# Kernel optimization log

Measured on AMD Instinct MI355X. Metric: run time of the kernel, lower is better.

Reference implementation:

```python
import jax, jax.numpy as jnp
import numpy as np

HIDDEN = 4096
N_HEADS = 32
N_KV = 8
HEAD_DIM = 128
ROPE_BASE = 10000.0


def setup_inputs() -> dict:
    key = jax.random.key(0)
    k0, k1, k2, k3, k4 = jax.random.split(key, 5)
    B, S = 1, 2048
    scale = 0.02
    return {
        "hidden_states": jax.random.normal(k0, (B, S, HIDDEN), dtype=jnp.float32),
        "Wq": jax.random.normal(k1, (N_HEADS * HEAD_DIM, HIDDEN), dtype=jnp.float32) * scale,
        "Wk": jax.random.normal(k2, (N_KV * HEAD_DIM, HIDDEN), dtype=jnp.float32) * scale,
        "Wv": jax.random.normal(k3, (N_KV * HEAD_DIM, HIDDEN), dtype=jnp.float32) * scale,
        "Wo": jax.random.normal(k4, (HIDDEN, N_HEADS * HEAD_DIM), dtype=jnp.float32) * scale,
    }


def _rotate_half(x):
    x1, x2 = jnp.split(x, 2, axis=-1)
    return jnp.concatenate([-x2, x1], axis=-1)


def _rope_cos_sin(seq_len, dtype):
    inv_freq = 1.0 / (ROPE_BASE ** (jnp.arange(0, HEAD_DIM, 2, dtype=jnp.float32) / HEAD_DIM))
    t = jnp.arange(seq_len, dtype=jnp.float32)
    freqs = jnp.outer(t, inv_freq)                 # [S, hd/2]
    emb = jnp.concatenate([freqs, freqs], axis=-1) # [S, hd]
    return jnp.cos(emb).astype(dtype), jnp.sin(emb).astype(dtype)


def reference(hidden_states, Wq, Wk, Wv, Wo):
    B, S, _ = hidden_states.shape
    scale = HEAD_DIM ** -0.5
    groups = N_HEADS // N_KV

    q = (hidden_states @ Wq.T).reshape(B, S, N_HEADS, HEAD_DIM).transpose(0, 2, 1, 3)
    k = (hidden_states @ Wk.T).reshape(B, S, N_KV, HEAD_DIM).transpose(0, 2, 1, 3)
    v = (hidden_states @ Wv.T).reshape(B, S, N_KV, HEAD_DIM).transpose(0, 2, 1, 3)

    cos, sin = _rope_cos_sin(S, q.dtype)           # [S, hd] each, broadcast over (B, H)
    q = q * cos + _rotate_half(q) * sin
    k = k * cos + _rotate_half(k) * sin

    # repeat_kv: [B, nkv, S, hd] -> [B, nkv*groups, S, hd]
    k = jnp.broadcast_to(k[:, :, None], (B, N_KV, groups, S, HEAD_DIM)).reshape(B, N_HEADS, S, HEAD_DIM)
    v = jnp.broadcast_to(v[:, :, None], (B, N_KV, groups, S, HEAD_DIM)).reshape(B, N_HEADS, S, HEAD_DIM)

    scores = jnp.einsum('bhqd,bhkd->bhqk', q, k) * scale
    causal = jnp.tril(jnp.ones((S, S), dtype=bool))
    scores = jnp.where(causal, scores, -jnp.inf)
    probs = jax.nn.softmax(scores.astype(jnp.float32), axis=-1).astype(q.dtype)

    attn = jnp.einsum('bhqk,bhkd->bhqd', probs, v)            # [B, H, S, hd]
    attn = attn.transpose(0, 2, 1, 3).reshape(B, S, N_HEADS * HEAD_DIM)
    return attn @ Wo.T
```

## Files before the change

### kernel.cpp

```cpp
#include <hip/hip_runtime.h>
#include <hip/hip_bf16.h>
#include <math.h>

#define S_LEN 2048
#define HIDDEN 4096
#define N_HEADS 32
#define N_KV 8
#define HEAD_DIM 128

typedef __attribute__((ext_vector_type(8))) short short8;
typedef __attribute__((ext_vector_type(4))) float f32x4;

typedef __attribute__((address_space(3))) unsigned int as3_u32;
typedef const __attribute__((address_space(1))) unsigned int as1_u32;

__device__ __forceinline__ void gload16(const void* g, void* lds) {
  __builtin_amdgcn_global_load_lds((as1_u32*)g, (as3_u32*)lds, 16, 0, 0);
}

__device__ __forceinline__ unsigned short f2bf(float f) {
  unsigned int u = __float_as_uint(f);
  return (unsigned short)((u + 0x7fff + ((u >> 16) & 1)) >> 16);
}
__device__ __forceinline__ float bf2f(unsigned short u) {
  return __uint_as_float(((unsigned int)u) << 16);
}

__global__ void conv_bf16(const float* __restrict__ in, unsigned short* __restrict__ out, int n) {
  int i = (blockIdx.x * blockDim.x + threadIdx.x) * 4;
  if (i >= n) return;
  float4 v = *(const float4*)&in[i];
  ushort4 o;
  o.x = f2bf(v.x); o.y = f2bf(v.y); o.z = f2bf(v.z); o.w = f2bf(v.w);
  *(ushort4*)&out[i] = o;
}

__device__ __forceinline__ void storeC(float* C, float v) { *C = v; }
__device__ __forceinline__ void storeC(unsigned short* C, float v) { *C = f2bf(v); }

#define BM 256
#define BN 128

#define BK2 32
#define NKT2 (HIDDEN / BK2)

__global__ __launch_bounds__(512, 4) void gemm_qkv(
    const unsigned short* __restrict__ Xb,
    const unsigned short* __restrict__ Wqb, const unsigned short* __restrict__ Wkb,
    const unsigned short* __restrict__ Wvb,
    unsigned short* __restrict__ Qb, unsigned short* __restrict__ Kb,
    unsigned short* __restrict__ Vb) {
  const int colBase = blockIdx.x * BN;
  const int rowBase = blockIdx.y * BM;
  const unsigned short* Bw;
  unsigned short* Cb;
  int ldc, ccol;
  if (colBase < 4096)      { Bw = Wqb + (size_t)colBase * HIDDEN;          Cb = Qb; ldc = 4096; ccol = colBase; }
  else if (colBase < 5120) { Bw = Wkb + (size_t)(colBase - 4096) * HIDDEN; Cb = Kb; ldc = 1024; ccol = colBase - 4096; }
  else                     { Bw = Wvb + (size_t)(colBase - 5120) * HIDDEN; Cb = Vb; ldc = 1024; ccol = colBase - 5120; }
  const unsigned short* A = Xb + (size_t)rowBase * HIDDEN;
  unsigned short* C = Cb + (size_t)rowBase * ldc + ccol;

  __shared__ unsigned short Abuf[3][BM * BK2];
  __shared__ unsigned short Bbuf[3][BN * BK2];

  const int tid = threadIdx.x;
  const int w = tid >> 6;
  const int lane = tid & 63;
  const int lrow = lane & 15;
  const int lk8 = lane >> 4;
  const int wr = (w >> 1) * 64;
  const int wc = (w & 1) * 64;
  const int lr16 = lane >> 2;
  const int lp = lane & 3;

  f32x4 acc[4][4];
#pragma unroll
  for (int i = 0; i < 4; i++)
#pragma unroll
    for (int j = 0; j < 4; j++) acc[i][j] = (f32x4){0.f, 0.f, 0.f, 0.f};

#define STAGE_A2(bi, t, g) {                                                   \
    int seg = (g) * 8 + w;                                          \
    int r = seg * 16 + lr16;                                                   \
    int c = lp ^ (r & 3);                                                      \
    gload16(&A[(size_t)r * HIDDEN + (t) * BK2 + c * 8], &Abuf[bi][seg * 512]); \
  }
#define STAGE_B2(bi, t) {                                                      \
    int seg = w;                                                     \
    int r = seg * 16 + lr16;                                                   \
    int c = lp ^ (r & 3);                                                      \
    gload16(&Bw[(size_t)r * HIDDEN + (t) * BK2 + c * 8], &Bbuf[bi][seg * 512]);\
  }
#define RD_FRAG2(buf, rbase)                                                   \
  (*(const short8*)&(buf)[((rbase) + lrow) * 32 + ((lk8) ^ (((rbase) + lrow) & 3)) * 8])

  STAGE_A2(0, 0, 0); STAGE_A2(0, 0, 1); STAGE_B2(0, 0);
  STAGE_A2(1, 1, 0); STAGE_A2(1, 1, 1); STAGE_B2(1, 1);
  asm volatile("s_waitcnt vmcnt(3)" ::: "memory");
  __builtin_amdgcn_s_barrier();

  for (int t = 0; t < NKT2; t++) {
    const int bi = t % 3;
    const int bs = (t + 2) % 3;
    const bool st = (t + 2) < NKT2;
    const unsigned short* Ac = Abuf[bi];
    const unsigned short* Bc = Bbuf[bi];

    short8 afr[4], bfr[4];
#pragma unroll
    for (int m = 0; m < 4; m++) afr[m] = RD_FRAG2(Ac, wr + m * 16);
#pragma unroll
    for (int n = 0; n < 4; n++) bfr[n] = RD_FRAG2(Bc, wc + n * 16);
    if (st) { STAGE_A2(bs, t + 2, 0); STAGE_A2(bs, t + 2, 1); STAGE_B2(bs, t + 2); }
    __builtin_amdgcn_s_barrier();
    __builtin_amdgcn_s_setprio(1);
#pragma unroll
    for (int m = 0; m < 4; m++)
#pragma unroll
      for (int n = 0; n < 4; n++)
        acc[m][n] = __builtin_amdgcn_mfma_f32_16x16x32_bf16(afr[m], bfr[n], acc[m][n], 0, 0, 0);
    __builtin_amdgcn_s_setprio(0);
    if (st) asm volatile("s_waitcnt vmcnt(3)" ::: "memory");
    else    asm volatile("s_waitcnt vmcnt(0)" ::: "memory");
    __builtin_amdgcn_s_barrier();
  }
#undef STAGE_A2
#undef STAGE_B2
#undef RD_FRAG2

#pragma unroll
  for (int i = 0; i < 4; i++)
#pragma unroll
    for (int j = 0; j < 4; j++) {
      int col = wc + j * 16 + lrow;
#pragma unroll
      for (int r = 0; r < 4; r++) {
        int row = wr + i * 16 + lk8 * 4 + r;
        storeC(&C[(size_t)row * ldc + col], acc[i][j][r]);
      }
    }
}

#define BK 64
#define NKT (HIDDEN / BK)

__global__ __launch_bounds__(512, 2) void gemm_out(
    const unsigned short* __restrict__ Ob, const unsigned short* __restrict__ Wob,
    float* __restrict__ C_) {
  const int colBase = blockIdx.x * BN;
  const int rowBase = blockIdx.y * BM;
  const unsigned short* A = Ob + (size_t)rowBase * HIDDEN;
  const unsigned short* B = Wob + (size_t)colBase * HIDDEN;
  float* C = C_ + (size_t)rowBase * HIDDEN + colBase;
  const int ldc = HIDDEN;

  __shared__ unsigned short Abuf[3][BM * BK];
  __shared__ unsigned short Bbuf[3][BN * BK];

  const int tid = threadIdx.x;
  const int w = tid >> 6;
  const int lane = tid & 63;
  const int lrow = lane & 15;
  const int lk8 = lane >> 4;
  const int wr = (w >> 1) * 64;
  const int wc = (w & 1) * 64;
  const int lr8 = lane >> 3;
  const int lp = lane & 7;

  f32x4 acc[4][4];
#pragma unroll
  for (int i = 0; i < 4; i++)
#pragma unroll
    for (int j = 0; j < 4; j++) acc[i][j] = (f32x4){0.f, 0.f, 0.f, 0.f};

#define STAGE_A(bi, t, g) {                                                  \
    int seg = (g) * 8 + w;                                                   \
    int r = seg * 8 + lr8;                                                   \
    int c = lp ^ (r & 7);                                                    \
    gload16(&A[(size_t)r * HIDDEN + (t) * BK + c * 8], &Abuf[bi][seg * 512]);\
  }
#define STAGE_B(bi, t, g) {                                                  \
    int seg = (g) * 8 + w;                                                   \
    int r = seg * 8 + lr8;                                                   \
    int c = lp ^ (r & 7);                                                    \
    gload16(&B[(size_t)r * HIDDEN + (t) * BK + c * 8], &Bbuf[bi][seg * 512]);\
  }
#define RD_FRAG(buf, rbase, ks)                                              \
  (*(const short8*)&(buf)[((rbase) + lrow) * 64 + (((ks) * 4 + lk8) ^ (((rbase) + lrow) & 7)) * 8])

#pragma unroll
  for (int g = 0; g < 4; g++) STAGE_A(0, 0, g);
#pragma unroll
  for (int g = 0; g < 2; g++) STAGE_B(0, 0, g);
#pragma unroll
  for (int g = 0; g < 4; g++) STAGE_A(1, 1, g);
#pragma unroll
  for (int g = 0; g < 2; g++) STAGE_B(1, 1, g);
  asm volatile("s_waitcnt vmcnt(6)" ::: "memory");
  __builtin_amdgcn_s_barrier();

  for (int t = 0; t < NKT; t++) {
    const int bi = t % 3;
    const int bs = (t + 2) % 3;
    const bool st = (t + 2) < NKT;
    const unsigned short* Ac = Abuf[bi];
    const unsigned short* Bc = Bbuf[bi];

    short8 bfr[4][2], afr[2][2];

#pragma unroll
    for (int n = 0; n < 4; n++)
#pragma unroll
      for (int ks = 0; ks < 2; ks++)
        bfr[n][ks] = RD_FRAG(Bc, wc + n * 16, ks);
#pragma unroll
    for (int m = 0; m < 2; m++)
#pragma unroll
      for (int ks = 0; ks < 2; ks++)
        afr[m][ks] = RD_FRAG(Ac, wr + m * 16, ks);
    if (st) { STAGE_A(bs, t + 2, 0); STAGE_A(bs, t + 2, 1); STAGE_B(bs, t + 2, 0); }
    __builtin_amdgcn_s_barrier();
    __builtin_amdgcn_s_setprio(1);
#pragma unroll
    for (int m = 0; m < 2; m++)
#pragma unroll
      for (int n = 0; n < 4; n++)
#pragma unroll
        for (int ks = 0; ks < 2; ks++)
          acc[m][n] = __builtin_amdgcn_mfma_f32_16x16x32_bf16(afr[m][ks], bfr[n][ks], acc[m][n], 0, 0, 0);
    __builtin_amdgcn_s_setprio(0);
    __builtin_amdgcn_s_barrier();

#pragma unroll
    for (int m = 0; m < 2; m++)
#pragma unroll
      for (int ks = 0; ks < 2; ks++)
        afr[m][ks] = RD_FRAG(Ac, wr + (m + 2) * 16, ks);
    if (st) { STAGE_A(bs, t + 2, 2); STAGE_A(bs, t + 2, 3); STAGE_B(bs, t + 2, 1); }
    __builtin_amdgcn_s_barrier();
    __builtin_amdgcn_s_setprio(1);
#pragma unroll
    for (int m = 0; m < 2; m++)
#pragma unroll
      for (int n = 0; n < 4; n++)
#pragma unroll
        for (int ks = 0; ks < 2; ks++)
          acc[m + 2][n] = __builtin_amdgcn_mfma_f32_16x16x32_bf16(afr[m][ks], bfr[n][ks], acc[m + 2][n], 0, 0, 0);
    __builtin_amdgcn_s_setprio(0);
    if (st) asm volatile("s_waitcnt vmcnt(6)" ::: "memory");
    else    asm volatile("s_waitcnt vmcnt(0)" ::: "memory");
    __builtin_amdgcn_s_barrier();
  }
#undef STAGE_A
#undef STAGE_B
#undef RD_FRAG

#pragma unroll
  for (int i = 0; i < 4; i++)
#pragma unroll
    for (int j = 0; j < 4; j++) {
      int col = wc + j * 16 + lrow;
#pragma unroll
      for (int r = 0; r < 4; r++) {
        int row = wr + i * 16 + lk8 * 4 + r;
        storeC(&C[(size_t)row * ldc + col], acc[i][j][r]);
      }
    }
}

#define QSCALE 0.12753102123752056f

__global__ void rope_kernel(const unsigned short* __restrict__ Q,
                            const unsigned short* __restrict__ K,
                            unsigned short* __restrict__ Qp,
                            unsigned short* __restrict__ Kp) {
  int idx = blockIdx.x * blockDim.x + threadIdx.x;
  int d = idx & 63;
  int sh = idx >> 6;
  int h = sh % (N_HEADS + N_KV);
  int s = sh / (N_HEADS + N_KV);
  if (s >= S_LEN) return;

  float freq = expf(-(float)d * (9.210340371976184f / 64.0f));
  float ang = (float)s * freq;
  float sn, cs;
  sincosf(ang, &sn, &cs);

  const unsigned short* src;
  unsigned short* dst;
  float sc_out;
  if (h < N_HEADS) {
    src = Q + ((size_t)s * N_HEADS + h) * HEAD_DIM;
    dst = Qp + (((size_t)h * 128 + (s >> 4)) * 16 + (s & 15)) * HEAD_DIM;
    sc_out = QSCALE;
  } else {
    int kvh = h - N_HEADS;
    src = K + ((size_t)s * N_KV + kvh) * HEAD_DIM;
    dst = Kp + (((size_t)kvh * 32 + (s >> 6)) * 64 + (s & 63)) * HEAD_DIM;
    sc_out = 1.0f;
  }

  float x1 = bf2f(src[d]);
  float x2 = bf2f(src[d + 64]);
  dst[d] = f2bf((x1 * cs - x2 * sn) * sc_out);
  dst[d + 64] = f2bf((x2 * cs + x1 * sn) * sc_out);
}

__global__ __launch_bounds__(256) void transp_v(
    const unsigned short* __restrict__ Vb, unsigned short* __restrict__ Vp) {
  __shared__ unsigned short t[64][72];
  const int s0 = blockIdx.x * 64;
  const int c0 = blockIdx.y * 64;
  const int kt = s0 >> 6;
  const int tid = threadIdx.x;
#pragma unroll
  for (int i = 0; i < 2; i++) {
    int c = tid + i * 256;
    int r = c >> 3, ch = c & 7;
    *(short8*)&t[r][ch * 8] = *(const short8*)&Vb[(size_t)(s0 + r) * 1024 + c0 + ch * 8];
  }
  __syncthreads();
#pragma unroll
  for (int i = 0; i < 4; i++) {
    int c = tid + i * 256;
    int orow = c >> 4, oc4 = (c & 15) * 4;
    int g = c0 + orow;
    int kvh = g >> 7, d = g & 127;
    ushort4 o;
    o.x = t[oc4 + 0][orow]; o.y = t[oc4 + 1][orow];
    o.z = t[oc4 + 2][orow]; o.w = t[oc4 + 3][orow];
    *(ushort4*)&Vp[(((size_t)kvh * 32 + kt) * 128 + d) * 64 + oc4] = o;
  }
}

#define AK 64

__global__ __launch_bounds__(256, 4) void attn_mfma(
    const unsigned short* __restrict__ Qp, const unsigned short* __restrict__ Kp,
    const unsigned short* __restrict__ Vp, unsigned short* __restrict__ Ob) {
  const int b = blockIdx.x;
  const int h = b & 31;
  const int j = b >> 5;
  const int qt = (b < 512) ? j : (47 - j);
  const int kvh = h >> 2;

  const int tid = threadIdx.x;
  const int w = tid >> 6;
  const int lane = tid & 63;
  const int lrow = lane & 15;
  const int lk8 = lane >> 4;

  __shared__ unsigned short Ks[64 * 128];
  __shared__ unsigned short Vts[128 * 64];
  __shared__ unsigned short Ps[4 * 16 * 64];
  unsigned short* Pw = &Ps[w * 16 * 64];

  short8 qf[4];
  const int t0 = qt * 4 + w;
#pragma unroll
  for (int ks = 0; ks < 4; ks++)
    qf[ks] = *(const short8*)&Qp[(((size_t)h * 128 + t0) * 16 + lrow) * 128 +
                                 ks * 32 + lk8 * 8];

  f32x4 acc[8];
  float m_i = -1e30f, l_i = 0.f;
#pragma unroll
  for (int n = 0; n < 8; n++) acc[n] = (f32x4){0.f, 0.f, 0.f, 0.f};

  const int nkt = qt + 1;

  for (int kt = 0; kt < nkt; kt++) {
    const int kb = kt * AK;
    const unsigned short* Kt  = Kp + ((size_t)kvh * 32 + kt) * 8192;
    const unsigned short* Vtt = Vp + ((size_t)kvh * 32 + kt) * 8192;

    __syncthreads();
#pragma unroll
    for (int jj = 0; jj < 4; jj++) {
      int seg = w * 4 + jj;
      int kr = seg * 4 + lk8;
      int kc = lrow ^ (kr & 15);
      gload16(Kt + ((size_t)kr * 16 + kc) * 8, &Ks[seg * 512]);
      int vr = seg * 8 + (lane >> 3);
      int vc = (lane & 7) ^ (vr & 7);
      gload16(Vtt + ((size_t)vr * 8 + vc) * 8, &Vts[seg * 512]);
    }
    __syncthreads();

    f32x4 s[4];
#pragma unroll
    for (int n = 0; n < 4; n++) s[n] = (f32x4){0.f, 0.f, 0.f, 0.f};

#pragma unroll
    for (int ks = 0; ks < 4; ks++) {
      short8 kf[4];
#pragma unroll
      for (int n = 0; n < 4; n++)
        kf[n] = *(const short8*)&Ks[(n * 16 + lrow) * 128 + (((ks * 4 + lk8) ^ lrow)) * 8];
#pragma unroll
      for (int n = 0; n < 4; n++)
        s[n] = __builtin_amdgcn_mfma_f32_16x16x32_bf16(kf[n], qf[ks], s[n], 0, 0, 0);
    }

    const int wqb = qt * 64 + w * 16;
    if (kb + AK - 1 > wqb) {
      int query = wqb + lrow;
#pragma unroll
      for (int n = 0; n < 4; n++) {
        int keyb = kb + n * 16 + lk8 * 4;
#pragma unroll
        for (int r = 0; r < 4; r++)
          if (keyb + r > query) s[n][r] = -1e30f;
      }
    }

    {
      float mx = -1e30f;
#pragma unroll
      for (int n = 0; n < 4; n++)
#pragma unroll
        for (int r = 0; r < 4; r++) mx = fmaxf(mx, s[n][r]);
      mx = fmaxf(mx, __shfl_xor(mx, 16, 64));
      mx = fmaxf(mx, __shfl_xor(mx, 32, 64));
      float mn = fmaxf(m_i, mx);
      float al = exp2f(m_i - mn);
      m_i = mn;
      float ls = 0.f;
#pragma unroll
      for (int n = 0; n < 4; n++)
#pragma unroll
        for (int r = 0; r < 4; r++) {
          float e = exp2f(s[n][r] - mn);
          s[n][r] = e;
          ls += e;
        }
      ls += __shfl_xor(ls, 16, 64);
      ls += __shfl_xor(ls, 32, 64);
      l_i = l_i * al + ls;
#pragma unroll
      for (int n = 0; n < 8; n++)
#pragma unroll
        for (int r = 0; r < 4; r++) acc[n][r] *= al;
    }

#pragma unroll
    for (int n = 0; n < 4; n++) {
      ushort4 pk;
      pk.x = f2bf(s[n][0]); pk.y = f2bf(s[n][1]);
      pk.z = f2bf(s[n][2]); pk.w = f2bf(s[n][3]);
      int c8 = n * 4 + lk8;
      int c16s = (c8 >> 1) ^ (lrow & 7);
      *(ushort4*)&Pw[lrow * 64 + c16s * 8 + (c8 & 1) * 4] = pk;
    }

#pragma unroll
    for (int ks2 = 0; ks2 < 2; ks2++) {
      int c16s = (ks2 * 4 + lk8) ^ (lrow & 7);
      short8 pf = *(const short8*)&Pw[lrow * 64 + c16s * 8];
#pragma unroll
      for (int n = 0; n < 8; n++) {
        short8 vf = *(const short8*)&Vts[(n * 16 + lrow) * 64 +
                                         (((ks2 * 4 + lk8) ^ (lrow & 7))) * 8];
        acc[n] = __builtin_amdgcn_mfma_f32_16x16x32_bf16(vf, pf, acc[n], 0, 0, 0);
      }
    }
  }

  {
    float inv = 1.0f / l_i;
    int row = qt * 64 + w * 16 + lrow;
#pragma unroll
    for (int n = 0; n < 8; n++) {
      ushort4 o;
      o.x = f2bf(acc[n][0] * inv); o.y = f2bf(acc[n][1] * inv);
      o.z = f2bf(acc[n][2] * inv); o.w = f2bf(acc[n][3] * inv);
      *(ushort4*)&Ob[(size_t)row * 4096 + h * 128 + n * 16 + lk8 * 4] = o;
    }
  }
}

extern "C" void kernel_launch(void* const* d_in, const int* in_sizes, int n_in,
                              void* d_out, int out_size, void* d_ws, size_t ws_size,
                              hipStream_t stream) {
  const float* X  = (const float*)d_in[0];
  const float* Wq = (const float*)d_in[1];
  const float* Wk = (const float*)d_in[2];
  const float* Wv = (const float*)d_in[3];
  const float* Wo = (const float*)d_in[4];
  float* out = (float*)d_out;

  char* p = (char*)d_ws;
  unsigned short* Qb  = (unsigned short*)p; p += (size_t)S_LEN * 4096 * 2;
  unsigned short* Kb  = (unsigned short*)p; p += (size_t)S_LEN * 1024 * 2;
  unsigned short* Vb  = (unsigned short*)p; p += (size_t)S_LEN * 1024 * 2;
  unsigned short* Qp  = (unsigned short*)p; p += (size_t)S_LEN * 4096 * 2;
  unsigned short* Kp  = (unsigned short*)p; p += (size_t)S_LEN * 1024 * 2;
  unsigned short* Vp  = (unsigned short*)p; p += (size_t)S_LEN * 1024 * 2;
  unsigned short* Xb  = (unsigned short*)p; p += (size_t)S_LEN * 4096 * 2;
  unsigned short* Wqb = (unsigned short*)p; p += (size_t)4096 * 4096 * 2;
  unsigned short* Wkb = (unsigned short*)p; p += (size_t)1024 * 4096 * 2;
  unsigned short* Wvb = (unsigned short*)p; p += (size_t)1024 * 4096 * 2;
  unsigned short* Ob  = Xb;
  unsigned short* Wob = Wqb;

  conv_bf16<<<(S_LEN * 4096 / 4 + 255) / 256, 256, 0, stream>>>(X, Xb, S_LEN * 4096);
  conv_bf16<<<(4096 * 4096 / 4 + 255) / 256, 256, 0, stream>>>(Wq, Wqb, 4096 * 4096);
  conv_bf16<<<(1024 * 4096 / 4 + 255) / 256, 256, 0, stream>>>(Wk, Wkb, 1024 * 4096);
  conv_bf16<<<(1024 * 4096 / 4 + 255) / 256, 256, 0, stream>>>(Wv, Wvb, 1024 * 4096);

  gemm_qkv<<<dim3(6144 / BN, S_LEN / BM), 512, 0, stream>>>(Xb, Wqb, Wkb, Wvb, Qb, Kb, Vb);

  int rope_threads = S_LEN * (N_HEADS + N_KV) * 64;
  rope_kernel<<<rope_threads / 256, 256, 0, stream>>>(Qb, Kb, Qp, Kp);

  transp_v<<<dim3(S_LEN / 64, 1024 / 64), 256, 0, stream>>>(Vb, Vp);

  conv_bf16<<<(4096 * 4096 / 4 + 255) / 256, 256, 0, stream>>>(Wo, Wob, 4096 * 4096);

  attn_mfma<<<1024, 256, 0, stream>>>(Qp, Kp, Vp, Ob);

  gemm_out<<<dim3(4096 / BN, S_LEN / BM), 512, 0, stream>>>(Ob, Wob, out);
}
```

Measured before the change: 475.3 us.

## Fuse conversion and prep kernels, shrink QKV GEMM tile to 128x128

Merges the four fp32-to-bf16 conversions into one launch, and RoPE, the V transpose and the Wo conversion into a second, cutting the host launch count. Separately, the QKV GEMM drops from 256x128 tiles with 512 threads to 128x128 tiles with 256 threads. That doubles the grid to 768 blocks, which should fill the CUs better, at the cost of re-reading each weight tile more often. Fusing also makes the Wo conversion wait for the QKV GEMM instead of running independently.

```diff
diff --git a/kernel.cpp b/kernel.cpp
--- a/kernel.cpp
+++ b/kernel.cpp
@@ -26,32 +26,39 @@
   return __uint_as_float(((unsigned int)u) << 16);
 }
 
-__global__ void conv_bf16(const float* __restrict__ in, unsigned short* __restrict__ out, int n) {
-  int i = (blockIdx.x * blockDim.x + threadIdx.x) * 4;
-  if (i >= n) return;
-  float4 v = *(const float4*)&in[i];
+__device__ __forceinline__ void storeC(float* C, float v) { *C = v; }
+__device__ __forceinline__ void storeC(unsigned short* C, float v) { *C = f2bf(v); }
+
+__global__ __launch_bounds__(256) void conv4(
+    const float* __restrict__ X, const float* __restrict__ Wq,
+    const float* __restrict__ Wk, const float* __restrict__ Wv,
+    unsigned short* __restrict__ Xb, unsigned short* __restrict__ Wqb,
+    unsigned short* __restrict__ Wkb, unsigned short* __restrict__ Wvb) {
+  size_t i = ((size_t)blockIdx.x * 256 + threadIdx.x) * 4;
+  const float* src; unsigned short* dst; size_t off;
+  if (i < 8388608UL)       { src = X;  dst = Xb;  off = i; }
+  else if (i < 25165824UL) { src = Wq; dst = Wqb; off = i - 8388608UL; }
+  else if (i < 29360128UL) { src = Wk; dst = Wkb; off = i - 25165824UL; }
+  else                     { src = Wv; dst = Wvb; off = i - 29360128UL; }
+  float4 v = *(const float4*)&src[off];
   ushort4 o;
   o.x = f2bf(v.x); o.y = f2bf(v.y); o.z = f2bf(v.z); o.w = f2bf(v.w);
-  *(ushort4*)&out[i] = o;
-}
-
-__device__ __forceinline__ void storeC(float* C, float v) { *C = v; }
-__device__ __forceinline__ void storeC(unsigned short* C, float v) { *C = f2bf(v); }
-
-#define BM 256
+  *(ushort4*)&dst[off] = o;
+}
+
 #define BN 128
 
 #define BK2 32
 #define NKT2 (HIDDEN / BK2)
 
-__global__ __launch_bounds__(512, 4) void gemm_qkv(
+__global__ __launch_bounds__(256, 3) void gemm_qkv(
     const unsigned short* __restrict__ Xb,
     const unsigned short* __restrict__ Wqb, const unsigned short* __restrict__ Wkb,
     const unsigned short* __restrict__ Wvb,
     unsigned short* __restrict__ Qb, unsigned short* __restrict__ Kb,
     unsigned short* __restrict__ Vb) {
   const int colBase = blockIdx.x * BN;
-  const int rowBase = blockIdx.y * BM;
+  const int rowBase = blockIdx.y * 128;
   const unsigned short* Bw;
   unsigned short* Cb;
   int ldc, ccol;
@@ -61,7 +68,7 @@
   const unsigned short* A = Xb + (size_t)rowBase * HIDDEN;
   unsigned short* C = Cb + (size_t)rowBase * ldc + ccol;
 
-  __shared__ unsigned short Abuf[3][BM * BK2];
+  __shared__ unsigned short Abuf[3][128 * BK2];
   __shared__ unsigned short Bbuf[3][BN * BK2];
 
   const int tid = threadIdx.x;
@@ -81,13 +88,13 @@
     for (int j = 0; j < 4; j++) acc[i][j] = (f32x4){0.f, 0.f, 0.f, 0.f};
 
 #define STAGE_A2(bi, t, g) {                                                   \
-    int seg = (g) * 8 + w;                                          \
+    int seg = (g) * 4 + w;                                           \
     int r = seg * 16 + lr16;                                                   \
     int c = lp ^ (r & 3);                                                      \
     gload16(&A[(size_t)r * HIDDEN + (t) * BK2 + c * 8], &Abuf[bi][seg * 512]); \
   }
-#define STAGE_B2(bi, t) {                                                      \
-    int seg = w;                                                     \
+#define STAGE_B2(bi, t, g) {                                                   \
+    int seg = (g) * 4 + w;                                           \
     int r = seg * 16 + lr16;                                                   \
     int c = lp ^ (r & 3);                                                      \
     gload16(&Bw[(size_t)r * HIDDEN + (t) * BK2 + c * 8], &Bbuf[bi][seg * 512]);\
@@ -95,9 +102,9 @@
 #define RD_FRAG2(buf, rbase)                                                   \
   (*(const short8*)&(buf)[((rbase) + lrow) * 32 + ((lk8) ^ (((rbase) + lrow) & 3)) * 8])
 
-  STAGE_A2(0, 0, 0); STAGE_A2(0, 0, 1); STAGE_B2(0, 0);
-  STAGE_A2(1, 1, 0); STAGE_A2(1, 1, 1); STAGE_B2(1, 1);
-  asm volatile("s_waitcnt vmcnt(3)" ::: "memory");
+  STAGE_A2(0, 0, 0); STAGE_A2(0, 0, 1); STAGE_B2(0, 0, 0); STAGE_B2(0, 0, 1);
+  STAGE_A2(1, 1, 0); STAGE_A2(1, 1, 1); STAGE_B2(1, 1, 0); STAGE_B2(1, 1, 1);
+  asm volatile("s_waitcnt vmcnt(4)" ::: "memory");
   __builtin_amdgcn_s_barrier();
 
   for (int t = 0; t < NKT2; t++) {
@@ -112,7 +119,8 @@
     for (int m = 0; m < 4; m++) afr[m] = RD_FRAG2(Ac, wr + m * 16);
 #pragma unroll
     for (int n = 0; n < 4; n++) bfr[n] = RD_FRAG2(Bc, wc + n * 16);
-    if (st) { STAGE_A2(bs, t + 2, 0); STAGE_A2(bs, t + 2, 1); STAGE_B2(bs, t + 2); }
+    if (st) { STAGE_A2(bs, t + 2, 0); STAGE_A2(bs, t + 2, 1);
+              STAGE_B2(bs, t + 2, 0); STAGE_B2(bs, t + 2, 1); }
     __builtin_amdgcn_s_barrier();
     __builtin_amdgcn_s_setprio(1);
 #pragma unroll
@@ -121,7 +129,7 @@
       for (int n = 0; n < 4; n++)
         acc[m][n] = __builtin_amdgcn_mfma_f32_16x16x32_bf16(afr[m], bfr[n], acc[m][n], 0, 0, 0);
     __builtin_amdgcn_s_setprio(0);
-    if (st) asm volatile("s_waitcnt vmcnt(3)" ::: "memory");
+    if (st) asm volatile("s_waitcnt vmcnt(4)" ::: "memory");
     else    asm volatile("s_waitcnt vmcnt(0)" ::: "memory");
     __builtin_amdgcn_s_barrier();
   }
@@ -142,6 +150,7 @@
     }
 }
 
+#define BM 256
 #define BK 64
 #define NKT (HIDDEN / BK)
 
@@ -270,68 +279,85 @@
 }
 
 #define QSCALE 0.12753102123752056f
-
-__global__ void rope_kernel(const unsigned short* __restrict__ Q,
-                            const unsigned short* __restrict__ K,
-                            unsigned short* __restrict__ Qp,
-                            unsigned short* __restrict__ Kp) {
-  int idx = blockIdx.x * blockDim.x + threadIdx.x;
-  int d = idx & 63;
-  int sh = idx >> 6;
-  int h = sh % (N_HEADS + N_KV);
-  int s = sh / (N_HEADS + N_KV);
-  if (s >= S_LEN) return;
-
-  float freq = expf(-(float)d * (9.210340371976184f / 64.0f));
-  float ang = (float)s * freq;
-  float sn, cs;
-  sincosf(ang, &sn, &cs);
-
-  const unsigned short* src;
-  unsigned short* dst;
-  float sc_out;
-  if (h < N_HEADS) {
-    src = Q + ((size_t)s * N_HEADS + h) * HEAD_DIM;
-    dst = Qp + (((size_t)h * 128 + (s >> 4)) * 16 + (s & 15)) * HEAD_DIM;
-    sc_out = QSCALE;
-  } else {
-    int kvh = h - N_HEADS;
-    src = K + ((size_t)s * N_KV + kvh) * HEAD_DIM;
-    dst = Kp + (((size_t)kvh * 32 + (s >> 6)) * 64 + (s & 63)) * HEAD_DIM;
-    sc_out = 1.0f;
-  }
-
-  float x1 = bf2f(src[d]);
-  float x2 = bf2f(src[d + 64]);
-  dst[d] = f2bf((x1 * cs - x2 * sn) * sc_out);
-  dst[d + 64] = f2bf((x2 * cs + x1 * sn) * sc_out);
-}
-
-__global__ __launch_bounds__(256) void transp_v(
-    const unsigned short* __restrict__ Vb, unsigned short* __restrict__ Vp) {
+#define ROPE_BLOCKS 20480
+#define TR_BLOCKS 512
+
+__global__ __launch_bounds__(256) void prep_fused(
+    const unsigned short* __restrict__ Qb, const unsigned short* __restrict__ Kb,
+    const unsigned short* __restrict__ Vb,
+    unsigned short* __restrict__ Qp, unsigned short* __restrict__ Kp,
+    unsigned short* __restrict__ Vp,
+    const float* __restrict__ Wo, unsigned short* __restrict__ Wob) {
   __shared__ unsigned short t[64][72];
-  const int s0 = blockIdx.x * 64;
-  const int c0 = blockIdx.y * 64;
-  const int kt = s0 >> 6;
   const int tid = threadIdx.x;
-#pragma unroll
-  for (int i = 0; i < 2; i++) {
-    int c = tid + i * 256;
-    int r = c >> 3, ch = c & 7;
-    *(short8*)&t[r][ch * 8] = *(const short8*)&Vb[(size_t)(s0 + r) * 1024 + c0 + ch * 8];
-  }
-  __syncthreads();
-#pragma unroll
-  for (int i = 0; i < 4; i++) {
-    int c = tid + i * 256;
-    int orow = c >> 4, oc4 = (c & 15) * 4;
-    int g = c0 + orow;
-    int kvh = g >> 7, d = g & 127;
-    ushort4 o;
-    o.x = t[oc4 + 0][orow]; o.y = t[oc4 + 1][orow];
-    o.z = t[oc4 + 2][orow]; o.w = t[oc4 + 3][orow];
-    *(ushort4*)&Vp[(((size_t)kvh * 32 + kt) * 128 + d) * 64 + oc4] = o;
-  }
+  int bx = blockIdx.x;
+
+  if (bx < ROPE_BLOCKS) {
+    int idx = bx * 256 + tid;
+    int d = idx & 63;
+    int sh = idx >> 6;
+    int h = sh % (N_HEADS + N_KV);
+    int s = sh / (N_HEADS + N_KV);
+    if (s >= S_LEN) return;
+
+    float freq = expf(-(float)d * (9.210340371976184f / 64.0f));
+    float ang = (float)s * freq;
+    float sn, cs;
+    sincosf(ang, &sn, &cs);
+
+    const unsigned short* src;
+    unsigned short* dst;
+    float sc_out;
+    if (h < N_HEADS) {
+      src = Qb + ((size_t)s * N_HEADS + h) * HEAD_DIM;
+      dst = Qp + (((size_t)h * 128 + (s >> 4)) * 16 + (s & 15)) * HEAD_DIM;
+      sc_out = QSCALE;
+    } else {
+      int kvh = h - N_HEADS;
+      src = Kb + ((size_t)s * N_KV + kvh) * HEAD_DIM;
+      dst = Kp + (((size_t)kvh * 32 + (s >> 6)) * 64 + (s & 63)) * HEAD_DIM;
+      sc_out = 1.0f;
+    }
+
+    float x1 = bf2f(src[d]);
+    float x2 = bf2f(src[d + 64]);
+    dst[d] = f2bf((x1 * cs - x2 * sn) * sc_out);
+    dst[d + 64] = f2bf((x2 * cs + x1 * sn) * sc_out);
+    return;
+  }
+  bx -= ROPE_BLOCKS;
+
+  if (bx < TR_BLOCKS) {
+    const int s0 = (bx & 31) * 64;
+    const int c0 = (bx >> 5) * 64;
+    const int kt = s0 >> 6;
+#pragma unroll
+    for (int i = 0; i < 2; i++) {
+      int c = tid + i * 256;
+      int r = c >> 3, ch = c & 7;
+      *(short8*)&t[r][ch * 8] = *(const short8*)&Vb[(size_t)(s0 + r) * 1024 + c0 + ch * 8];
+    }
+    __syncthreads();
+#pragma unroll
+    for (int i = 0; i < 4; i++) {
+      int c = tid + i * 256;
+      int orow = c >> 4, oc4 = (c & 15) * 4;
+      int g = c0 + orow;
+      int kvh = g >> 7, d = g & 127;
+      ushort4 o;
+      o.x = t[oc4 + 0][orow]; o.y = t[oc4 + 1][orow];
+      o.z = t[oc4 + 2][orow]; o.w = t[oc4 + 3][orow];
+      *(ushort4*)&Vp[(((size_t)kvh * 32 + kt) * 128 + d) * 64 + oc4] = o;
+    }
+    return;
+  }
+  bx -= TR_BLOCKS;
+
+  size_t i = ((size_t)bx * 256 + tid) * 4;
+  float4 v = *(const float4*)&Wo[i];
+  ushort4 o;
+  o.x = f2bf(v.x); o.y = f2bf(v.y); o.z = f2bf(v.z); o.w = f2bf(v.w);
+  *(ushort4*)&Wob[i] = o;
 }
 
 #define AK 64
@@ -504,19 +530,12 @@
   unsigned short* Ob  = Xb;
   unsigned short* Wob = Wqb;
 
-  conv_bf16<<<(S_LEN * 4096 / 4 + 255) / 256, 256, 0, stream>>>(X, Xb, S_LEN * 4096);
-  conv_bf16<<<(4096 * 4096 / 4 + 255) / 256, 256, 0, stream>>>(Wq, Wqb, 4096 * 4096);
-  conv_bf16<<<(1024 * 4096 / 4 + 255) / 256, 256, 0, stream>>>(Wk, Wkb, 1024 * 4096);
-  conv_bf16<<<(1024 * 4096 / 4 + 255) / 256, 256, 0, stream>>>(Wv, Wvb, 1024 * 4096);
-
-  gemm_qkv<<<dim3(6144 / BN, S_LEN / BM), 512, 0, stream>>>(Xb, Wqb, Wkb, Wvb, Qb, Kb, Vb);
-
-  int rope_threads = S_LEN * (N_HEADS + N_KV) * 64;
-  rope_kernel<<<rope_threads / 256, 256, 0, stream>>>(Qb, Kb, Qp, Kp);
-
-  transp_v<<<dim3(S_LEN / 64, 1024 / 64), 256, 0, stream>>>(Vb, Vp);
-
-  conv_bf16<<<(4096 * 4096 / 4 + 255) / 256, 256, 0, stream>>>(Wo, Wob, 4096 * 4096);
+  conv4<<<32768, 256, 0, stream>>>(X, Wq, Wk, Wv, Xb, Wqb, Wkb, Wvb);
+
+  gemm_qkv<<<dim3(6144 / BN, S_LEN / 128), 256, 0, stream>>>(Xb, Wqb, Wkb, Wvb, Qb, Kb, Vb);
+
+  prep_fused<<<ROPE_BLOCKS + TR_BLOCKS + 16384, 256, 0, stream>>>(
+      Qb, Kb, Vb, Qp, Kp, Vp, Wo, Wob);
 
   attn_mfma<<<1024, 256, 0, stream>>>(Qp, Kp, Vp, Ob);
 
```

Measured after the change: 475.4 us. About the same (+0.0%).
